# Kernel optimization log

Measured on AMD Instinct MI355X. Metric: run time of the kernel, lower is better.

## Reference

```python
import jax, jax.numpy as jnp
import numpy as np


def setup_inputs() -> dict:
    key = jax.random.key(0)
    ks = jax.random.split(key, 7)
    t, e, h = 2048, 512, 8
    s = 0.02
    return {
        "x": jax.random.normal(ks[0], (t, e), jnp.float32),
        "y": jax.random.normal(ks[1], (t, e), jnp.float32),
        "Wk": jax.random.normal(ks[2], (e, e * h), jnp.float32) * s,
        "Wq": jax.random.normal(ks[3], (e, e * h), jnp.float32) * s,
        "Wv": jax.random.normal(ks[4], (e, e * h), jnp.float32) * s,
        "Wu": jax.random.normal(ks[5], (e * h, e), jnp.float32) * s,
        "bu": jnp.zeros((e,), jnp.float32),
    }


def reference(x, y, Wk, Wq, Wv, Wu, bu):
    t, e = x.shape
    h = Wk.shape[1] // e
    scale = e ** (-0.25)
    # projections -> [h, t, e] (head dim equals emb in this 'wide' attention)
    k = (x @ Wk).reshape(t, h, e).transpose(1, 0, 2) * scale
    q = (y @ Wq).reshape(t, h, e).transpose(1, 0, 2) * scale
    v = (x @ Wv).reshape(t, h, e).transpose(1, 0, 2)
    # scores [h, t, t]
    dot = jnp.einsum('hte,hse->hts', q, k)
    attn = jax.nn.softmax(dot, axis=-1)
    out = jnp.einsum('hts,hse->hte', attn, v)          # [h, t, e]
    out = out.transpose(1, 0, 2).reshape(t, h * e)     # [t, h*e]
    return (out @ Wu + bu)[None]                       # [1, t, e] (b=1 in original)
```

## Files before the change

### kernel.cpp

```cpp
#include <hip/hip_runtime.h>
#include <hip/hip_bf16.h>
#include <stdint.h>

#define T_SEQ 2048
#define EMB   512
#define NH    8
#define HEAD_ALL 4096

typedef __attribute__((ext_vector_type(8))) short short8;
typedef __attribute__((ext_vector_type(4))) float f32x4;

__device__ __forceinline__ unsigned short f2b(float f) {
    __hip_bfloat16 h = __float2bfloat16(f);
    return *reinterpret_cast<unsigned short*>(&h);
}
__device__ __forceinline__ float b2f(unsigned short u) {
    return __uint_as_float(((unsigned)u) << 16);
}
__device__ __forceinline__ void gload_lds16(const void* g, void* l) {
    __builtin_amdgcn_global_load_lds((__attribute__((address_space(1))) void*)(void*)(g),
                                     (__attribute__((address_space(3))) void*)(l), 16, 0, 0);
}
__device__ __forceinline__ void wg_barrier() {
    asm volatile("" ::: "memory");
    __builtin_amdgcn_s_barrier();
    asm volatile("" ::: "memory");
}

__global__ void cvt_bf16_2(const float* __restrict__ a, const float* __restrict__ b,
                           unsigned short* __restrict__ oa, unsigned short* __restrict__ ob, int n8) {
    const float* in = blockIdx.y ? b : a;
    unsigned short* out = blockIdx.y ? ob : oa;
    int i = blockIdx.x * 256 + threadIdx.x;
    if (i >= n8) return;
    const f32x4* p = (const f32x4*)in + 2 * (size_t)i;
    f32x4 va = p[0], vb = p[1];
    uint4 o;
    o.x = (unsigned)f2b(va[0]) | ((unsigned)f2b(va[1]) << 16);
    o.y = (unsigned)f2b(va[2]) | ((unsigned)f2b(va[3]) << 16);
    o.z = (unsigned)f2b(vb[0]) | ((unsigned)f2b(vb[1]) << 16);
    o.w = (unsigned)f2b(vb[2]) | ((unsigned)f2b(vb[3]) << 16);
    *((uint4*)out + i) = o;
}

__global__ void transpose_cvt3_f32(const float* __restrict__ w0, const float* __restrict__ w1,
                                   const float* __restrict__ w2, unsigned short* __restrict__ out,
                                   int R, int C, long outS) {
    __shared__ unsigned short t[64][66];
    const int z = blockIdx.z;
    const float* in = (z == 0) ? w0 : ((z == 1) ? w1 : w2);
    unsigned short* ob = out + (long)z * outS;
    const int tid = threadIdx.x;
    const int r0 = blockIdx.y * 64, c0 = blockIdx.x * 64;
#pragma unroll
    for (int it = 0; it < 4; ++it) {
        int flat = it * 256 + tid;
        int r = flat >> 4, c4 = flat & 15;
        f32x4 v = *(const f32x4*)(in + (long)(r0 + r) * C + c0 + c4 * 4);
#pragma unroll
        for (int w = 0; w < 4; ++w) t[r][c4 * 4 + w] = f2b(v[w]);
    }
    __syncthreads();
#pragma unroll
    for (int it = 0; it < 2; ++it) {
        int flat = it * 256 + tid;
        int rr = flat >> 3, c8 = flat & 7;
        unsigned u[4];
#pragma unroll
        for (int w = 0; w < 4; ++w) {
            unsigned short a = t[c8 * 8 + 2 * w][rr];
            unsigned short b = t[c8 * 8 + 2 * w + 1][rr];
            u[w] = (unsigned)a | ((unsigned)b << 16);
        }
        *(uint4*)(ob + (long)(c0 + rr) * R + r0 + c8 * 8) = make_uint4(u[0], u[1], u[2], u[3]);
    }
}

__global__ void transpose_bf16(const unsigned short* __restrict__ in, unsigned short* __restrict__ out,
                               int R, int C, long inS, long outS) {
    __shared__ unsigned short t[64][66];
    const unsigned short* ib = in + (long)blockIdx.z * inS;
    unsigned short* ob = out + (long)blockIdx.z * outS;
    const int tid = threadIdx.x;
    const int r0 = blockIdx.y * 64, c0 = blockIdx.x * 64;
#pragma unroll
    for (int it = 0; it < 2; ++it) {
        int flat = it * 256 + tid;
        int r = flat >> 3, c8 = flat & 7;
        uint4 v = *(const uint4*)(ib + (long)(r0 + r) * C + c0 + c8 * 8);
        unsigned u[4] = {v.x, v.y, v.z, v.w};
#pragma unroll
        for (int w = 0; w < 4; ++w) {
            t[r][c8 * 8 + 2 * w]     = (unsigned short)(u[w] & 0xffff);
            t[r][c8 * 8 + 2 * w + 1] = (unsigned short)(u[w] >> 16);
        }
    }
    __syncthreads();
#pragma unroll
    for (int it = 0; it < 2; ++it) {
        int flat = it * 256 + tid;
        int rr = flat >> 3, c8 = flat & 7;
        unsigned u[4];
#pragma unroll
        for (int w = 0; w < 4; ++w)
            u[w] = (unsigned)t[c8 * 8 + 2 * w][rr] | ((unsigned)t[c8 * 8 + 2 * w + 1][rr] << 16);
        *(uint4*)(ob + (long)(c0 + rr) * R + r0 + c8 * 8) = make_uint4(u[0], u[1], u[2], u[3]);
    }
}

template<int R_>
__device__ __forceinline__ void stage2(const unsigned short* __restrict__ src, int kfull,
                                       short* ldsbase, int i, int tid, int wid) {
#pragma unroll
    for (int s = 0; s < 2; ++s) {
        const int ii = i + s;
        const int r = ii * 64 + (tid >> 3);
        const int d = (tid & 7) * 16;
        const int sc = (d ^ ((r & 7) << 4)) >> 1;
        gload_lds16(src + (long)r * kfull + sc, ldsbase + ii * 4096 + wid * 512);
    }
}

template<int BM, int BN, int KTILES, int MODE>
__global__ __launch_bounds__(512, 2)
void gemm8p(const unsigned short* __restrict__ A, const unsigned short* __restrict__ A2,
            const unsigned short* __restrict__ B, void* __restrict__ Cout,
            float* __restrict__ rpart,
            int kfull, float alpha, long As, long Bs, long Cs, int ldc)
{
    static_assert(KTILES >= 3, "pipeline needs >=3 K-tiles");
    constexpr int ATILE = BM * 64;
    constexpr int BTILE = BN * 64;
    constexpr int LA = BM / 64;
    constexpr int LB = BN / 64;
    constexpr int MF = BM / 32;
    constexpr int NF = BN / 64;
    constexpr int MFP = MF / 4;
    constexpr int LDSN = 2 * (ATILE + BTILE);

    __shared__ __align__(16) short lds[LDSN + ((MODE == 4) ? 2 * BM : 0)];

    const int tid = threadIdx.x;
    const int wid = tid >> 6, lane = tid & 63;
    const int wm = wid >> 2, wn = wid & 3;
    const int fr = lane & 15, fq = lane >> 4;

    const int nwg = gridDim.x * gridDim.y * gridDim.z;
    int flat = blockIdx.x + gridDim.x * (blockIdx.y + gridDim.y * blockIdx.z);
    flat = (flat & 7) * (nwg >> 3) + (flat >> 3);
    const int bx = flat % gridDim.x;
    const int rem = flat / gridDim.x;
    const int by = rem % gridDim.y;
    const long batch = rem / gridDim.y;

    const int bm = by * BM, bn = bx * BN;

    const unsigned short* Ab;
    const unsigned short* Bb;
    int koff = 0;
    if constexpr (MODE == 1) { Ab = (batch == 2) ? A2 : A; Bb = B + batch * Bs; }
    else if constexpr (MODE == 3) { Ab = A; Bb = B; koff = (int)batch * (KTILES * 64); }
    else { Ab = A + batch * As; Bb = B + batch * Bs; }

    const unsigned short* Ag = Ab + (long)bm * kfull + koff;
    const unsigned short* Bg = Bb + (long)bn * kfull + koff;

    f32x4 acc[MF][NF];
#pragma unroll
    for (int i = 0; i < MF; i++)
#pragma unroll
        for (int j = 0; j < NF; j++) acc[i][j] = 0.f;

    float* rinv = (float*)(lds + LDSN);
    if constexpr (MODE == 4) {
        for (int r = tid; r < BM; r += 512) {
            float s = 0.f;
#pragma unroll
            for (int i = 0; i < 32; ++i) s += rpart[((long)batch * 32 + i) * T_SEQ + bm + r];
            rinv[r] = 1.0f / s;
        }
        asm volatile("s_waitcnt lgkmcnt(0)" ::: "memory");
    }

#pragma unroll
    for (int i = 0; i < LA; i += 2) stage2<BM>(Ag, kfull, lds, i, tid, wid);
#pragma unroll
    for (int i = 0; i < LB; i += 2) stage2<BN>(Bg, kfull, lds + 2 * ATILE, i, tid, wid);
#pragma unroll
    for (int i = 0; i < LB; i += 2) stage2<BN>(Bg + 64, kfull, lds + 2 * ATILE + BTILE, i, tid, wid);
    if constexpr (LB == 4) asm volatile("s_waitcnt vmcnt(4)" ::: "memory");
    else                   asm volatile("s_waitcnt vmcnt(2)" ::: "memory");
    wg_barrier();

#pragma unroll 2
    for (int t = 0; t < KTILES; ++t) {
        short* la  = lds + (t & 1) * ATILE;
        short* laN = lds + ((t + 1) & 1) * ATILE;
        short* lb  = lds + 2 * ATILE + (t & 1) * BTILE;
        const int kA = (t + 1) * 64;
        const int kB = (t + 2) * 64;

        short8 bfrag[NF][2];
#pragma unroll
        for (int q = 0; q < 4; ++q) {
            if (q == 0) {
#pragma unroll
                for (int nf = 0; nf < NF; ++nf)
#pragma unroll
                    for (int kk = 0; kk < 2; ++kk) {
                        const int r = wn * (BN / 4) + nf * 16 + fr;
                        const int cb = kk * 64 + fq * 16;
                        bfrag[nf][kk] = *(const short8*)(lb + r * 64 + ((cb ^ ((r & 7) << 4)) >> 1));
                    }
            }
            short8 afrag[MFP][2];
#pragma unroll
            for (int mf = 0; mf < MFP; ++mf)
#pragma unroll
                for (int kk = 0; kk < 2; ++kk) {
                    const int r = wm * (BM / 2) + q * (BM / 8) + mf * 16 + fr;
                    const int cb = kk * 64 + fq * 16;
                    afrag[mf][kk] = *(const short8*)(la + r * 64 + ((cb ^ ((r & 7) << 4)) >> 1));
                }
            if (t + 1 < KTILES) {
                if (q == 0) stage2<BM>(Ag + kA, kfull, laN, 0, tid, wid);
                if (q == 1 && LA == 4) stage2<BM>(Ag + kA, kfull, laN, 2, tid, wid);
            }
            if (t + 2 < KTILES) {
                if (q == 2) stage2<BN>(Bg + kB, kfull, lb, 0, tid, wid);
                if (q == 3 && LB == 4) stage2<BN>(Bg + kB, kfull, lb, 2, tid, wid);
            }
            wg_barrier();
            __builtin_amdgcn_s_setprio(1);
#pragma unroll
            for (int mf = 0; mf < MFP; ++mf)
#pragma unroll
                for (int nf = 0; nf < NF; ++nf)
#pragma unroll
                    for (int kk = 0; kk < 2; ++kk)
                        acc[q * MFP + mf][nf] = __builtin_amdgcn_mfma_f32_16x16x32_bf16(
                            afrag[mf][kk], bfrag[nf][kk], acc[q * MFP + mf][nf], 0, 0, 0);
            __builtin_amdgcn_s_setprio(0);
            if (q == 3) {
                if (t + 2 < KTILES) {
                    if constexpr (LB == 4) asm volatile("s_waitcnt vmcnt(4)" ::: "memory");
                    else                   asm volatile("s_waitcnt vmcnt(2)" ::: "memory");
                } else {
                    asm volatile("s_waitcnt vmcnt(0)" ::: "memory");
                }
            }
            wg_barrier();
        }
    }

#pragma unroll
    for (int m = 0; m < MF; ++m)
#pragma unroll
        for (int j = 0; j < 4; ++j) {
            const int row = bm + wm * (BM / 2) + m * 16 + fq * 4 + j;
            float rowsum = 0.f;
#pragma unroll
            for (int n = 0; n < NF; ++n) {
                const int col = bn + wn * (BN / 4) + n * 16 + fr;
                const float v = acc[m][n][j] * alpha;
                if constexpr (MODE == 1) {
                    unsigned short* C = (unsigned short*)Cout + batch * Cs;
                    C[(long)(col >> 9) * ((long)T_SEQ * EMB) + (long)row * EMB + (col & 511)] = f2b(v);
                } else if constexpr (MODE == 2) {
                    unsigned short* C = (unsigned short*)Cout + batch * Cs;
                    const unsigned short us = f2b(__expf(v));
                    C[(long)row * ldc + col] = us;
                    rowsum += b2f(us);
                } else if constexpr (MODE == 3) {
                    float* C = (float*)Cout + batch * ((long)T_SEQ * EMB);
                    C[(long)row * ldc + col] = v;
                } else {
                    unsigned short* C = (unsigned short*)Cout + batch * Cs;
                    C[(long)row * ldc + col] = f2b(v * rinv[row - bm]);
                }
            }
            if constexpr (MODE == 2) {
                rowsum += __shfl_xor(rowsum, 1);
                rowsum += __shfl_xor(rowsum, 2);
                rowsum += __shfl_xor(rowsum, 4);
                rowsum += __shfl_xor(rowsum, 8);
                if (fr == 0)
                    rpart[(((long)batch * 8 + bx) * 4 + wn) * T_SEQ + row] = rowsum;
            }
        }
}

__global__ void reduce_bias(const float* __restrict__ part, const float* __restrict__ bias,
                            float* __restrict__ out) {
    const int i = blockIdx.x * 256 + threadIdx.x;
    const long stride4 = (long)T_SEQ * EMB / 4;
    const f32x4* p = (const f32x4*)part;
    f32x4 s = p[i];
#pragma unroll
    for (int sl = 1; sl < 8; ++sl) s += p[i + sl * stride4];
    f32x4 b = *(const f32x4*)(bias + ((i * 4) % EMB));
    *((f32x4*)out + i) = s + b;
}

extern "C" void kernel_launch(void* const* d_in, const int* in_sizes, int n_in,
                              void* d_out, int out_size, void* d_ws, size_t ws_size,
                              hipStream_t stream)
{
    const float* x  = (const float*)d_in[0];
    const float* y  = (const float*)d_in[1];
    const float* Wk = (const float*)d_in[2];
    const float* Wq = (const float*)d_in[3];
    const float* Wv = (const float*)d_in[4];
    const float* Wu = (const float*)d_in[5];
    const float* bu = (const float*)d_in[6];
    char* ws = (char*)d_ws;
    const size_t MB = 1024ull * 1024ull;

    unsigned short* Sb   = (unsigned short*)(ws + 0);
    unsigned short* xb   = (unsigned short*)(ws + 0);
    unsigned short* yb   = (unsigned short*)(ws + 2 * MB);
    unsigned short* WT3  = (unsigned short*)(ws + 4 * MB);
    unsigned short* PRJ  = (unsigned short*)(ws + 48 * MB);
    unsigned short* Vb   = (unsigned short*)(ws + 48 * MB);
    unsigned short* WuT  = (unsigned short*)(ws + 96 * MB);
    unsigned short* VTb  = (unsigned short*)(ws + 100 * MB);
    unsigned short* Ob   = (unsigned short*)(ws + 116 * MB);
    float*          rpart= (float*)(ws + 132 * MB);
    float*          part = (float*)(ws + 0);
    unsigned short* Kb   = (unsigned short*)(ws + 64 * MB);
    unsigned short* Qb   = (unsigned short*)(ws + 80 * MB);

    const float scale2 = 0.04419417382415922f;
    const long TE = (long)T_SEQ * EMB;

    cvt_bf16_2<<<dim3(512, 2), dim3(256), 0, stream>>>(x, y, xb, yb, T_SEQ * EMB / 8);
    transpose_cvt3_f32<<<dim3(HEAD_ALL / 64, EMB / 64, 3), dim3(256), 0, stream>>>(
        Wv, Wk, Wq, WT3, EMB, HEAD_ALL, (long)2 * MB);
    transpose_cvt3_f32<<<dim3(EMB / 64, HEAD_ALL / 64, 1), dim3(256), 0, stream>>>(
        Wu, nullptr, nullptr, WuT, HEAD_ALL, EMB, 0);

    gemm8p<256, 256, 8, 1><<<dim3(HEAD_ALL / 256, T_SEQ / 256, 3), 512, 0, stream>>>(
        xb, yb, WT3, PRJ, nullptr, EMB, 1.f, 0, (long)2 * MB, (long)8 * MB, 0);

    transpose_bf16<<<dim3(EMB / 64, T_SEQ / 64, NH), dim3(256), 0, stream>>>(
        Vb, VTb, T_SEQ, EMB, TE, TE);

    gemm8p<256, 256, 8, 2><<<dim3(T_SEQ / 256, T_SEQ / 256, NH), 512, 0, stream>>>(
        Qb, nullptr, Kb, Sb, rpart, EMB, scale2, TE, TE, (long)T_SEQ * T_SEQ, T_SEQ);

    gemm8p<128, 256, 32, 4><<<dim3(EMB / 256, T_SEQ / 128, NH), 512, 0, stream>>>(
        Sb, nullptr, VTb, Ob, rpart, T_SEQ, 1.f, (long)T_SEQ * T_SEQ, TE, (long)EMB, HEAD_ALL);

    gemm8p<256, 128, 8, 3><<<dim3(EMB / 128, T_SEQ / 256, 8), 512, 0, stream>>>(
        Ob, nullptr, WuT, part, nullptr, HEAD_ALL, 1.f, 0, 0, 0, EMB);

    reduce_bias<<<dim3(T_SEQ * EMB / 4 / 256), dim3(256), 0, stream>>>(part, bu, (float*)d_out);
}
```

Baseline: 175.5 us.

## Fuse QK^T, exp and PV into single flash-style attention kernel

Replaces the separate score GEMM (writing exp'd bf16 scores plus row-sum partials to global memory) and the normalising PV GEMM with one kernel per (head, 64-query block). It keeps Q in registers and streams K and V^T tiles through LDS. Scores are exponentiated in registers and staged in LDS for the PV product, with normalisation applied at the end. This removes the roughly 64 MB of score traffic and one launch. The costs are only 256 workgroups, a large LDS footprint limiting occupancy, and no max subtraction (as before).

```diff
diff --git a/kernel.cpp b/kernel.cpp
--- a/kernel.cpp
+++ b/kernel.cpp
@@ -125,7 +125,6 @@
 __global__ __launch_bounds__(512, 2)
 void gemm8p(const unsigned short* __restrict__ A, const unsigned short* __restrict__ A2,
             const unsigned short* __restrict__ B, void* __restrict__ Cout,
-            float* __restrict__ rpart,
             int kfull, float alpha, long As, long Bs, long Cs, int ldc)
 {
     static_assert(KTILES >= 3, "pipeline needs >=3 K-tiles");
@@ -136,9 +135,8 @@
     constexpr int MF = BM / 32;
     constexpr int NF = BN / 64;
     constexpr int MFP = MF / 4;
-    constexpr int LDSN = 2 * (ATILE + BTILE);
-
-    __shared__ __align__(16) short lds[LDSN + ((MODE == 4) ? 2 * BM : 0)];
+
+    __shared__ __align__(16) short lds[2 * (ATILE + BTILE)];
 
     const int tid = threadIdx.x;
     const int wid = tid >> 6, lane = tid & 63;
@@ -159,8 +157,7 @@
     const unsigned short* Bb;
     int koff = 0;
     if constexpr (MODE == 1) { Ab = (batch == 2) ? A2 : A; Bb = B + batch * Bs; }
-    else if constexpr (MODE == 3) { Ab = A; Bb = B; koff = (int)batch * (KTILES * 64); }
-    else { Ab = A + batch * As; Bb = B + batch * Bs; }
+    else { Ab = A; Bb = B; koff = (int)batch * (KTILES * 64); }
 
     const unsigned short* Ag = Ab + (long)bm * kfull + koff;
     const unsigned short* Bg = Bb + (long)bn * kfull + koff;
@@ -170,17 +167,6 @@
     for (int i = 0; i < MF; i++)
 #pragma unroll
         for (int j = 0; j < NF; j++) acc[i][j] = 0.f;
-
-    float* rinv = (float*)(lds + LDSN);
-    if constexpr (MODE == 4) {
-        for (int r = tid; r < BM; r += 512) {
-            float s = 0.f;
-#pragma unroll
-            for (int i = 0; i < 32; ++i) s += rpart[((long)batch * 32 + i) * T_SEQ + bm + r];
-            rinv[r] = 1.0f / s;
-        }
-        asm volatile("s_waitcnt lgkmcnt(0)" ::: "memory");
-    }
 
 #pragma unroll
     for (int i = 0; i < LA; i += 2) stage2<BM>(Ag, kfull, lds, i, tid, wid);
@@ -258,7 +244,6 @@
 #pragma unroll
         for (int j = 0; j < 4; ++j) {
             const int row = bm + wm * (BM / 2) + m * 16 + fq * 4 + j;
-            float rowsum = 0.f;
 #pragma unroll
             for (int n = 0; n < NF; ++n) {
                 const int col = bn + wn * (BN / 4) + n * 16 + fr;
@@ -266,26 +251,154 @@
                 if constexpr (MODE == 1) {
                     unsigned short* C = (unsigned short*)Cout + batch * Cs;
                     C[(long)(col >> 9) * ((long)T_SEQ * EMB) + (long)row * EMB + (col & 511)] = f2b(v);
-                } else if constexpr (MODE == 2) {
-                    unsigned short* C = (unsigned short*)Cout + batch * Cs;
-                    const unsigned short us = f2b(__expf(v));
-                    C[(long)row * ldc + col] = us;
-                    rowsum += b2f(us);
-                } else if constexpr (MODE == 3) {
+                } else {
                     float* C = (float*)Cout + batch * ((long)T_SEQ * EMB);
                     C[(long)row * ldc + col] = v;
-                } else {
-                    unsigned short* C = (unsigned short*)Cout + batch * Cs;
-                    C[(long)row * ldc + col] = f2b(v * rinv[row - bm]);
                 }
             }
-            if constexpr (MODE == 2) {
-                rowsum += __shfl_xor(rowsum, 1);
-                rowsum += __shfl_xor(rowsum, 2);
-                rowsum += __shfl_xor(rowsum, 4);
-                rowsum += __shfl_xor(rowsum, 8);
-                if (fr == 0)
-                    rpart[(((long)batch * 8 + bx) * 4 + wn) * T_SEQ + row] = rowsum;
+        }
+}
+
+__global__ __launch_bounds__(512, 2)
+void attn_fused(const unsigned short* __restrict__ Qg, const unsigned short* __restrict__ Kg,
+                const unsigned short* __restrict__ VTg, unsigned short* __restrict__ Og,
+                float scale)
+{
+    __shared__ __align__(16) short lds[69888];
+    float* rs = (float*)(lds + 69632);
+    char* ldsb = (char*)lds;
+
+    const int tid = threadIdx.x;
+    const int wid = tid >> 6, lane = tid & 63;
+    const int fr = lane & 15, fq = lane >> 4;
+    const int rg = wid >> 1, ch = wid & 1;
+
+    const int orig = blockIdx.x + 32 * blockIdx.y;
+    const int f = (orig & 7) * 32 + (orig >> 3);
+    const int qb = f & 31, h = f >> 5;
+    const long TE = (long)T_SEQ * EMB;
+    const unsigned short* Qh = Qg + (long)h * TE + (long)(qb * 64) * EMB;
+    const unsigned short* Kh = Kg + (long)h * TE;
+    const unsigned short* Vh = VTg + (long)h * TE;
+
+    short8 qreg[16];
+#pragma unroll
+    for (int ks = 0; ks < 16; ++ks)
+        qreg[ks] = *(const short8*)(Qh + (long)(rg * 16 + fr) * EMB + ks * 32 + fq * 8);
+
+    auto stageK = [&](int kb) {
+#pragma unroll
+        for (int it = 0; it < 8; ++it) {
+            const int c = it * 512 + tid;
+            const int kv = c >> 6, s = c & 63;
+            gload_lds16(Kh + (long)(kb * 64 + kv) * EMB + (((s * 16) ^ ((kv & 7) << 4)) >> 1),
+                        lds + (it * 512 + wid * 64) * 8);
+        }
+    };
+    auto stageV = [&](int kb) {
+#pragma unroll
+        for (int it = 0; it < 8; ++it) {
+            const int c = it * 512 + tid;
+            const int d = c >> 3, s = c & 7;
+            gload_lds16(Vh + (long)d * T_SEQ + kb * 64 + (((s * 16) ^ ((d & 7) << 4)) >> 1),
+                        lds + 32768 + (it * 512 + wid * 64) * 8);
+        }
+    };
+
+    f32x4 oacc[4][4];
+#pragma unroll
+    for (int m = 0; m < 4; ++m)
+#pragma unroll
+        for (int n = 0; n < 4; ++n) oacc[m][n] = 0.f;
+    float rsum[4] = {0.f, 0.f, 0.f, 0.f};
+
+    stageK(0);
+    stageV(0);
+
+#pragma unroll 1
+    for (int t = 0; t < 32; ++t) {
+        asm volatile("s_waitcnt vmcnt(8)" ::: "memory");
+        wg_barrier();
+
+        f32x4 sacc[2][2];
+#pragma unroll
+        for (int c = 0; c < 2; ++c) { sacc[c][0] = 0.f; sacc[c][1] = 0.f; }
+#pragma unroll
+        for (int ks = 0; ks < 16; ++ks) {
+#pragma unroll
+            for (int c = 0; c < 2; ++c) {
+                const int kv = (ch * 2 + c) * 16 + fr;
+                const short8 bfr = *(const short8*)(ldsb + kv * 1024 +
+                                    (((ks * 64 + fq * 16)) ^ ((kv & 7) << 4)));
+                sacc[c][ks & 1] = __builtin_amdgcn_mfma_f32_16x16x32_bf16(
+                    qreg[ks], bfr, sacc[c][ks & 1], 0, 0, 0);
+            }
+        }
+#pragma unroll
+        for (int c = 0; c < 2; ++c)
+#pragma unroll
+            for (int j = 0; j < 4; ++j) {
+                const float v = __expf(scale * (sacc[c][0][j] + sacc[c][1][j]));
+                rsum[j] += v;
+                const int row = rg * 16 + fq * 4 + j;
+                const int kv = (ch * 2 + c) * 16 + fr;
+                *(unsigned short*)(ldsb + 131072 + row * 128 + ((kv * 2) ^ ((row & 7) << 4))) = f2b(v);
+            }
+        asm volatile("s_waitcnt lgkmcnt(0)" ::: "memory");
+        asm volatile("s_waitcnt vmcnt(0)" ::: "memory");
+        wg_barrier();
+        if (t + 1 < 32) stageK(t + 1);
+
+#pragma unroll
+        for (int kk = 0; kk < 2; ++kk) {
+            short8 sa[4], vb[4];
+#pragma unroll
+            for (int m = 0; m < 4; ++m) {
+                const int row = m * 16 + fr;
+                sa[m] = *(const short8*)(ldsb + 131072 + row * 128 +
+                          ((kk * 64 + fq * 16) ^ ((row & 7) << 4)));
+            }
+#pragma unroll
+            for (int n = 0; n < 4; ++n) {
+                const int d = wid * 64 + n * 16 + fr;
+                vb[n] = *(const short8*)(ldsb + 65536 + d * 128 +
+                          ((kk * 64 + fq * 16) ^ ((d & 7) << 4)));
+            }
+            __builtin_amdgcn_s_setprio(1);
+#pragma unroll
+            for (int m = 0; m < 4; ++m)
+#pragma unroll
+                for (int n = 0; n < 4; ++n)
+                    oacc[m][n] = __builtin_amdgcn_mfma_f32_16x16x32_bf16(
+                        sa[m], vb[n], oacc[m][n], 0, 0, 0);
+            __builtin_amdgcn_s_setprio(0);
+        }
+        wg_barrier();
+        if (t + 1 < 32) stageV(t + 1);
+    }
+
+#pragma unroll
+    for (int j = 0; j < 4; ++j) {
+        float v = rsum[j];
+        v += __shfl_xor(v, 1);
+        v += __shfl_xor(v, 2);
+        v += __shfl_xor(v, 4);
+        v += __shfl_xor(v, 8);
+        if (fr == 0) rs[ch * 64 + rg * 16 + fq * 4 + j] = v;
+    }
+    asm volatile("s_waitcnt lgkmcnt(0)" ::: "memory");
+    wg_barrier();
+
+#pragma unroll
+    for (int m = 0; m < 4; ++m)
+#pragma unroll
+        for (int j = 0; j < 4; ++j) {
+            const int row = m * 16 + fq * 4 + j;
+            const float rinv = 1.0f / (rs[row] + rs[64 + row]);
+#pragma unroll
+            for (int n = 0; n < 4; ++n) {
+                const int d = wid * 64 + n * 16 + fr;
+                Og[(long)(qb * 64 + row) * HEAD_ALL + h * EMB + d] = f2b(oacc[m][n][j] * rinv);
             }
         }
 }
@@ -316,19 +429,17 @@
     char* ws = (char*)d_ws;
     const size_t MB = 1024ull * 1024ull;
 
-    unsigned short* Sb   = (unsigned short*)(ws + 0);
     unsigned short* xb   = (unsigned short*)(ws + 0);
     unsigned short* yb   = (unsigned short*)(ws + 2 * MB);
     unsigned short* WT3  = (unsigned short*)(ws + 4 * MB);
     unsigned short* PRJ  = (unsigned short*)(ws + 48 * MB);
     unsigned short* Vb   = (unsigned short*)(ws + 48 * MB);
+    unsigned short* Kb   = (unsigned short*)(ws + 64 * MB);
+    unsigned short* Qb   = (unsigned short*)(ws + 80 * MB);
     unsigned short* WuT  = (unsigned short*)(ws + 96 * MB);
     unsigned short* VTb  = (unsigned short*)(ws + 100 * MB);
     unsigned short* Ob   = (unsigned short*)(ws + 116 * MB);
-    float*          rpart= (float*)(ws + 132 * MB);
     float*          part = (float*)(ws + 0);
-    unsigned short* Kb   = (unsigned short*)(ws + 64 * MB);
-    unsigned short* Qb   = (unsigned short*)(ws + 80 * MB);
 
     const float scale2 = 0.04419417382415922f;
     const long TE = (long)T_SEQ * EMB;
@@ -340,19 +451,15 @@
         Wu, nullptr, nullptr, WuT, HEAD_ALL, EMB, 0);
 
     gemm8p<256, 256, 8, 1><<<dim3(HEAD_ALL / 256, T_SEQ / 256, 3), 512, 0, stream>>>(
-        xb, yb, WT3, PRJ, nullptr, EMB, 1.f, 0, (long)2 * MB, (long)8 * MB, 0);
+        xb, yb, WT3, PRJ, EMB, 1.f, 0, (long)2 * MB, (long)8 * MB, 0);
 
     transpose_bf16<<<dim3(EMB / 64, T_SEQ / 64, NH), dim3(256), 0, stream>>>(
         Vb, VTb, T_SEQ, EMB, TE, TE);
 
-    gemm8p<256, 256, 8, 2><<<dim3(T_SEQ / 256, T_SEQ / 256, NH), 512, 0, stream>>>(
-        Qb, nullptr, Kb, Sb, rpart, EMB, scale2, TE, TE, (long)T_SEQ * T_SEQ, T_SEQ);
-
-    gemm8p<128, 256, 32, 4><<<dim3(EMB / 256, T_SEQ / 128, NH), 512, 0, stream>>>(
-        Sb, nullptr, VTb, Ob, rpart, T_SEQ, 1.f, (long)T_SEQ * T_SEQ, TE, (long)EMB, HEAD_ALL);
+    attn_fused<<<dim3(32, 8), 512, 0, stream>>>(Qb, Kb, VTb, Ob, scale2);
 
     gemm8p<256, 128, 8, 3><<<dim3(EMB / 128, T_SEQ / 256, 8), 512, 0, stream>>>(
-        Ob, nullptr, WuT, part, nullptr, HEAD_ALL, 1.f, 0, 0, 0, EMB);
+        Ob, nullptr, WuT, part, HEAD_ALL, 1.f, 0, 0, 0, EMB);
 
     reduce_bias<<<dim3(T_SEQ * EMB / 4 / 256), dim3(256), 0, stream>>>(part, bu, (float*)d_out);
 }
```

Result: slower. 181.2 us (+3.2%).
